# Optimization experiments

Measured on AMD Instinct MI355X. Metric: run time of the kernel, lower is better.

Reference implementation:

```python
import jax, jax.numpy as jnp
import numpy as np

B, N, D, H = 4, 2048, 512, 8
DK = D // H
NEG_SLOPE = 0.1


def setup_inputs() -> dict:
    key = jax.random.key(0)
    k_x, k_m, k_qkv, k_o, k_b = jax.random.split(key, 5)
    x = jax.random.normal(k_x, (B, N, D), dtype=jnp.float32)
    mask = jax.random.randint(k_m, (B, N, N), 0, 2).astype(bool)
    # guarantee self-edges so no row is fully masked (avoids NaN softmax)
    mask = mask | jnp.eye(N, dtype=bool)[None]
    scale = 1.0 / np.sqrt(D)
    Wqkv = jax.random.normal(k_qkv, (D, 3 * D), dtype=jnp.float32) * scale
    Wout = jax.random.normal(k_o, (D, D), dtype=jnp.float32) * scale
    bout = jax.random.normal(k_b, (D,), dtype=jnp.float32) * 0.01
    return {"x": x, "mask": mask, "Wqkv": Wqkv, "Wout": Wout, "bout": bout}


def reference(x, mask, Wqkv, Wout, bout):
    # x: (B,N,D), mask: (B,N,N) bool (True = keep edge)
    qkv = x @ Wqkv                               # (B,N,3D)
    q, k, v = jnp.split(qkv, 3, axis=-1)

    def heads(t):
        return t.reshape(B, N, H, DK).transpose(0, 2, 1, 3)  # (B,H,N,DK)

    q, k, v = heads(q), heads(k), heads(v)
    scores = jnp.einsum('bhnd,bhmd->bhnm', q, k) / np.sqrt(DK)  # (B,H,N,N)
    scores = jnp.where(mask[:, None], scores, -jnp.inf)
    attn = jax.nn.softmax(scores, axis=-1)
    out = jnp.einsum('bhnm,bhmd->bhnd', attn, v)               # (B,H,N,DK)
    out = out.transpose(0, 2, 1, 3).reshape(B, N, D)
    out = out @ Wout + bout
    return jnp.where(out >= 0, out, NEG_SLOPE * out)            # LeakyReLU
```

## Files before the change

kernel.cpp:

```cpp
#include <hip/hip_runtime.h>
#include <stdint.h>

#define Bb 4
#define Nn 2048
#define Dd 512
#define Hh 8
#define BN 8192

typedef __attribute__((ext_vector_type(4))) float f32x4;
typedef __attribute__((ext_vector_type(8))) short s16x8;

#define QSCALE 0.1803368801111204f

static constexpr size_t OFF_XB    = 1024;
static constexpr size_t OFF_WQKVT = OFF_XB    + (size_t)2 * BN * Dd;
static constexpr size_t OFF_WOUTT = OFF_WQKVT + (size_t)2 * 3 * Dd * Dd;
static constexpr size_t OFF_MASKP = OFF_WOUTT + (size_t)2 * Dd * Dd;
static constexpr size_t OFF_Q     = OFF_MASKP + (size_t)8 * Bb * Nn * (Nn / 64);
static constexpr size_t OFF_K     = OFF_Q     + (size_t)2 * BN * Dd;
static constexpr size_t OFF_VT    = OFF_K     + (size_t)2 * BN * Dd;
static constexpr size_t OFF_AO    = OFF_VT    + (size_t)2 * BN * Dd;

__device__ inline unsigned short f2bf(float f) {
  union { float f; unsigned int u; } v; v.f = f;
  const unsigned int u = v.u;
  return (unsigned short)((u + 0x7fffu + ((u >> 16) & 1u)) >> 16);
}

__device__ inline float exp2_hw(float x) {
  float r;
  asm("v_exp_f32 %0, %1" : "=v"(r) : "v"(x));
  return r;
}

__device__ inline unsigned int cvtpk_bf16(float lo, float hi) {
  unsigned int r;
  asm("v_cvt_pk_bf16_f32 %0, %1, %2" : "=v"(r) : "v"(lo), "v"(hi));
  return r;
}

__global__ void prep_kernel(const float* __restrict__ x, unsigned short* __restrict__ xb,
                            const float* __restrict__ Wqkv, unsigned short* __restrict__ wqkvT,
                            const float* __restrict__ Wout, unsigned short* __restrict__ woutT,
                            const unsigned char* __restrict__ mb, const int* __restrict__ mi,
                            unsigned long long* __restrict__ mp) {
  const int bid = blockIdx.x;
  if (bid < 2048) {
    for (int i = bid * 256 + threadIdx.x; i < BN * Dd / 4; i += 2048 * 256) {
      const float4 v = ((const float4*)x)[i];
      ushort4 o;
      o.x = f2bf(v.x); o.y = f2bf(v.y); o.z = f2bf(v.z); o.w = f2bf(v.w);
      ((ushort4*)xb)[i] = o;
    }
  } else if (bid < 3072) {
    for (int i = (bid - 2048) * 256 + threadIdx.x; i < Dd * 3 * Dd; i += 1024 * 256) {
      const int r = i / (3 * Dd), c = i - r * (3 * Dd);
      wqkvT[(size_t)c * Dd + r] = f2bf(Wqkv[i]);
    }
  } else if (bid < 3584) {
    for (int i = (bid - 3072) * 256 + threadIdx.x; i < Dd * Dd; i += 512 * 256) {
      const int r = i / Dd, c = i - r * Dd;
      woutT[(size_t)c * Dd + r] = f2bf(Wout[i]);
    }
  } else {
    const int lane = threadIdx.x & 63;
    const int ok = mb[(size_t)(lane + 1) * (Nn + 1)] != 0;
    const int bytemode = (__ballot(ok) == 0xFFFFFFFFFFFFFFFFull);
    const int nwords = Bb * Nn * (Nn / 64);
    int gw = ((bid - 3584) * 256 + threadIdx.x) >> 6;
    for (; gw < nwords; gw += 1024 * 4) {
      const size_t idx = (size_t)gw * 64 + lane;
      int v;
      if (bytemode) v = mb[idx]; else v = mi[idx];
      const unsigned long long bits = __ballot(v != 0);
      if (lane == 0) mp[gw] = bits;
    }
  }
}

template <int MODE>
__global__ __launch_bounds__(256, 2) void gemm128(
    const unsigned short* __restrict__ A,
    const unsigned short* __restrict__ BT,
    unsigned short* __restrict__ qb, unsigned short* __restrict__ kb,
    unsigned short* __restrict__ vt, const float* __restrict__ bias,
    float* __restrict__ outp) {
  __shared__ unsigned short Al[2][8192];
  __shared__ unsigned short Bl[2][8192];
  const int tid = threadIdx.x;
  const int lane = tid & 63, wv = tid >> 6;
  const int g = lane >> 4, n16 = lane & 15;
  const int m0 = blockIdx.x * 128;
  const int c0 = blockIdx.y * 128;
  const int wm = wv >> 1, wn = wv & 1;

  f32x4 acc[4][4] = {};

  auto stage = [&](int buf, int t) {
#pragma unroll
    for (int j = 0; j < 4; ++j) {
      const int base = (wv * 4 + j) * 1024;
      const int o = base + lane * 16;
      const int r = o >> 7;
      const int sl = ((o >> 4) & 7) ^ (r & 7);
      const unsigned short* ga = A + (size_t)(m0 + r) * 512 + t * 64 + sl * 8;
      __builtin_amdgcn_global_load_lds(
          (const __attribute__((address_space(1))) uint32_t*)ga,
          (__attribute__((address_space(3))) uint32_t*)&Al[buf][base / 2], 16, 0, 0);
      const unsigned short* gb = BT + (size_t)(c0 + r) * 512 + t * 64 + sl * 8;
      __builtin_amdgcn_global_load_lds(
          (const __attribute__((address_space(1))) uint32_t*)gb,
          (__attribute__((address_space(3))) uint32_t*)&Bl[buf][base / 2], 16, 0, 0);
    }
  };

  stage(0, 0);
  __syncthreads();
  int cur = 0;
  for (int t = 0; t < 8; ++t) {
    if (t < 7) stage(cur ^ 1, t + 1);
    s16x8 af[4][2], bfr[4][2];
#pragma unroll
    for (int f = 0; f < 4; ++f) {
#pragma unroll
      for (int kc = 0; kc < 2; ++kc) {
        const int rr = wm * 64 + f * 16 + n16;
        const int cc = wn * 64 + f * 16 + n16;
        const int sl = kc * 4 + g;
        af[f][kc]  = *(const s16x8*)&Al[cur][(rr * 128 + ((sl ^ (rr & 7)) * 16)) / 2];
        bfr[f][kc] = *(const s16x8*)&Bl[cur][(cc * 128 + ((sl ^ (cc & 7)) * 16)) / 2];
      }
    }
    __builtin_amdgcn_s_setprio(1);
#pragma unroll
    for (int i = 0; i < 4; ++i)
#pragma unroll
      for (int jn = 0; jn < 4; ++jn) {
        acc[i][jn] = __builtin_amdgcn_mfma_f32_16x16x32_bf16(af[i][0], bfr[jn][0], acc[i][jn], 0, 0, 0);
        acc[i][jn] = __builtin_amdgcn_mfma_f32_16x16x32_bf16(af[i][1], bfr[jn][1], acc[i][jn], 0, 0, 0);
      }
    __builtin_amdgcn_s_setprio(0);
    __syncthreads();
    cur ^= 1;
  }

  if (MODE == 0) {
#pragma unroll
    for (int i = 0; i < 4; ++i) {
      const int tok0 = m0 + wm * 64 + i * 16 + g * 4;
      const int bq = tok0 >> 11;
      const int nn0 = tok0 & 2047;
#pragma unroll
      for (int jn = 0; jn < 4; ++jn) {
        const int c = c0 + wn * 64 + jn * 16 + n16;
        if (c < 512) {
          const int h = c >> 6, dk = c & 63;
          unsigned short* qp = qb + (((size_t)bq * 8 + h) * 2048 + nn0) * 64 + dk;
#pragma unroll
          for (int r = 0; r < 4; ++r) qp[(size_t)r * 64] = f2bf(acc[i][jn][r] * QSCALE);
        } else if (c < 1024) {
          const int c2 = c - 512, h = c2 >> 6, dk = c2 & 63;
          unsigned short* kp = kb + (((size_t)bq * 8 + h) * 2048 + nn0) * 64 + dk;
#pragma unroll
          for (int r = 0; r < 4; ++r) kp[(size_t)r * 64] = f2bf(acc[i][jn][r]);
        } else {
          const int c2 = c - 1024, h = c2 >> 6, dk = c2 & 63;
          ushort4 pk;
          pk.x = f2bf(acc[i][jn][0]); pk.y = f2bf(acc[i][jn][1]);
          pk.z = f2bf(acc[i][jn][2]); pk.w = f2bf(acc[i][jn][3]);
          *(ushort4*)(vt + (((size_t)bq * 8 + h) * 64 + dk) * 2048 + nn0) = pk;
        }
      }
    }
  } else {
#pragma unroll
    for (int jn = 0; jn < 4; ++jn) {
      const int c = c0 + wn * 64 + jn * 16 + n16;
      const float bc = bias[c];
#pragma unroll
      for (int i = 0; i < 4; ++i) {
        const int tok0 = m0 + wm * 64 + i * 16 + g * 4;
#pragma unroll
        for (int r = 0; r < 4; ++r) {
          float v = acc[i][jn][r] + bc;
          v = v >= 0.f ? v : 0.1f * v;
          outp[(size_t)(tok0 + r) * 512 + c] = v;
        }
      }
    }
  }
}

__global__ __launch_bounds__(256, 4) void attn_kernel(
    const unsigned short* __restrict__ qb, const unsigned short* __restrict__ kb,
    const unsigned short* __restrict__ vt, const unsigned long long* __restrict__ mp,
    unsigned short* __restrict__ ao) {
  __shared__ unsigned short Kl[2][4096];
  __shared__ unsigned short Vl[2][4096];
  __shared__ unsigned short Pl[4][1024];
  const int tid = threadIdx.x, lane = tid & 63, wv = tid >> 6;
  const int g = lane >> 4, n16 = lane & 15;
  const int sbid = (blockIdx.x & 7) * 128 + (blockIdx.x >> 3);
  const int qt = sbid & 31, bh = sbid >> 5;
  const int b = bh >> 3, h = bh & 7;
  const int n0 = qt * 64 + wv * 16;
  const unsigned short* Qh = qb + (size_t)bh * 2048 * 64;
  const unsigned short* Kh = kb + (size_t)bh * 2048 * 64;
  const unsigned short* Vh = vt + (size_t)bh * 64 * 2048;
  const unsigned long long* mrow = mp + ((size_t)b * 2048 + n0 + n16) * 32;

  const s16x8 qf0 = *(const s16x8*)&Qh[(size_t)(n0 + n16) * 64 + g * 8];
  const s16x8 qf1 = *(const s16x8*)&Qh[(size_t)(n0 + n16) * 64 + 32 + g * 8];

  const s16x8 ones = {0x3F80, 0x3F80, 0x3F80, 0x3F80, 0x3F80, 0x3F80, 0x3F80, 0x3F80};

  f32x4 of[4] = {};
  f32x4 acc_l = {};

  unsigned short* Pw = Pl[wv];
  int pwo[4], pro[2];
#pragma unroll
  for (int mf = 0; mf < 4; ++mf) {
    int bo = n16 * 128 + mf * 32 + g * 8;
    pwo[mf] = bo ^ ((n16 & 7) << 4);
  }
#pragma unroll
  for (int kc = 0; kc < 2; ++kc) {
    int bo = n16 * 128 + kc * 64 + g * 16;
    pro[kc] = bo ^ ((n16 & 7) << 4);
  }

  auto stage = [&](int buf, int m0) {
#pragma unroll
    for (int j = 0; j < 2; ++j) {
      const int base = (wv * 2 + j) * 1024;
      const int o = base + lane * 16;
      const int r = o >> 7;
      const int sl = ((o >> 4) & 7) ^ (r & 7);
      const unsigned short* gk = Kh + (size_t)(m0 + r) * 64 + sl * 8;
      __builtin_amdgcn_global_load_lds(
          (const __attribute__((address_space(1))) uint32_t*)gk,
          (__attribute__((address_space(3))) uint32_t*)&Kl[buf][base / 2], 16, 0, 0);
      const unsigned short* gv = Vh + (size_t)r * 2048 + m0 + sl * 8;
      __builtin_amdgcn_global_load_lds(
          (const __attribute__((address_space(1))) uint32_t*)gv,
          (__attribute__((address_space(3))) uint32_t*)&Vl[buf][base / 2], 16, 0, 0);
    }
  };

  stage(0, 0);
  unsigned long long wbits = mrow[0];
  __syncthreads();
  int cur = 0;
  for (int it = 0; it < 32; ++it) {
    if (it < 31) stage(cur ^ 1, (it + 1) * 64);
    const unsigned long long wnext = (it < 31) ? mrow[it + 1] : 0ull;

    f32x4 sc[4] = {};
    __builtin_amdgcn_s_setprio(1);
#pragma unroll
    for (int mf = 0; mf < 4; ++mf) {
      const int ml = mf * 16 + n16;
#pragma unroll
      for (int kc = 0; kc < 2; ++kc) {
        const int sl = kc * 4 + g;
        const s16x8 kf = *(const s16x8*)&Kl[cur][(ml * 128 + ((sl ^ (ml & 7)) * 16)) / 2];
        sc[mf] = __builtin_amdgcn_mfma_f32_16x16x32_bf16(kf, kc ? qf1 : qf0, sc[mf], 0, 0, 0);
      }
    }
    __builtin_amdgcn_s_setprio(0);

    const unsigned int wlo = (unsigned int)(wbits >> (g * 4));
    const unsigned int whi = (unsigned int)(wbits >> (32 + g * 4));

    unsigned int w[8];
#pragma unroll
    for (int mf = 0; mf < 4; ++mf) {
      const unsigned int wsel = (mf & 2) ? whi : wlo;
      float p[4];
#pragma unroll
      for (int r = 0; r < 4; ++r) {
        const int bit = ((mf & 1) ? 16 : 0) + r;
        float pv = exp2_hw(sc[mf][r]);
        p[r] = (wsel & (1u << bit)) ? pv : 0.0f;
      }
      w[mf * 2]     = cvtpk_bf16(p[0], p[1]);
      w[mf * 2 + 1] = cvtpk_bf16(p[2], p[3]);
    }

#pragma unroll
    for (int mf = 0; mf < 4; ++mf) {
      uint2 pk2; pk2.x = w[mf * 2]; pk2.y = w[mf * 2 + 1];
      *(uint2*)((char*)Pw + pwo[mf]) = pk2;
    }
    __builtin_amdgcn_s_setprio(1);
#pragma unroll
    for (int kc = 0; kc < 2; ++kc) {
      const s16x8 pf = *(const s16x8*)((const char*)Pw + pro[kc]);
      acc_l = __builtin_amdgcn_mfma_f32_16x16x32_bf16(pf, ones, acc_l, 0, 0, 0);
#pragma unroll
      for (int df = 0; df < 4; ++df) {
        const int dk = df * 16 + n16;
        const int sl = kc * 4 + g;
        const s16x8 vf = *(const s16x8*)&Vl[cur][(dk * 128 + ((sl ^ (dk & 7)) * 16)) / 2];
        of[df] = __builtin_amdgcn_mfma_f32_16x16x32_bf16(pf, vf, of[df], 0, 0, 0);
      }
    }
    __builtin_amdgcn_s_setprio(0);
    wbits = wnext;
    __syncthreads();
    cur ^= 1;
  }

  float rinv[4];
#pragma unroll
  for (int r = 0; r < 4; ++r) rinv[r] = 1.f / acc_l[r];
#pragma unroll
  for (int df = 0; df < 4; ++df)
#pragma unroll
    for (int r = 0; r < 4; ++r) {
      const int token = b * 2048 + n0 + 4 * g + r;
      ao[(size_t)token * 512 + h * 64 + df * 16 + n16] = f2bf(of[df][r] * rinv[r]);
    }
}

extern "C" void kernel_launch(void* const* d_in, const int* in_sizes, int n_in,
                              void* d_out, int out_size, void* d_ws, size_t ws_size,
                              hipStream_t stream) {
  const float* x = (const float*)d_in[0];
  const void* mask = d_in[1];
  const float* Wqkv = (const float*)d_in[2];
  const float* Wout = (const float*)d_in[3];
  const float* bout = (const float*)d_in[4];
  float* out = (float*)d_out;
  char* ws = (char*)d_ws;

  unsigned short* xb = (unsigned short*)(ws + OFF_XB);
  unsigned short* wqkvT = (unsigned short*)(ws + OFF_WQKVT);
  unsigned short* woutT = (unsigned short*)(ws + OFF_WOUTT);
  unsigned long long* mp = (unsigned long long*)(ws + OFF_MASKP);
  unsigned short* qb = (unsigned short*)(ws + OFF_Q);
  unsigned short* kb = (unsigned short*)(ws + OFF_K);
  unsigned short* vt = (unsigned short*)(ws + OFF_VT);
  unsigned short* ao = (unsigned short*)(ws + OFF_AO);

  prep_kernel<<<4608, 256, 0, stream>>>(x, xb, Wqkv, wqkvT, Wout, woutT,
                                        (const unsigned char*)mask, (const int*)mask, mp);
  gemm128<0><<<dim3(64, 12), 256, 0, stream>>>(xb, wqkvT, qb, kb, vt, nullptr, nullptr);
  attn_kernel<<<1024, 256, 0, stream>>>(qb, kb, vt, mp, ao);
  gemm128<1><<<dim3(64, 4), 256, 0, stream>>>(ao, woutT, nullptr, nullptr, nullptr, bout, out);
}
```

Before: 129.7 us.

## Tile weight transposes via LDS, stage V-transpose epilogue, narrow out-proj tiles

```diff
diff --git a/kernel.cpp b/kernel.cpp
--- a/kernel.cpp
+++ b/kernel.cpp
@@ -39,35 +39,60 @@
   return r;
 }
 
+__device__ inline void gload16(const void* g, void* l) {
+  __builtin_amdgcn_global_load_lds(
+      (const __attribute__((address_space(1))) uint32_t*)g,
+      (__attribute__((address_space(3))) uint32_t*)l, 16, 0, 0);
+}
+
 __global__ void prep_kernel(const float* __restrict__ x, unsigned short* __restrict__ xb,
                             const float* __restrict__ Wqkv, unsigned short* __restrict__ wqkvT,
                             const float* __restrict__ Wout, unsigned short* __restrict__ woutT,
                             const unsigned char* __restrict__ mb, const int* __restrict__ mi,
                             unsigned long long* __restrict__ mp) {
-  const int bid = blockIdx.x;
+  __shared__ float tsm[64][65];
+  const int bid = blockIdx.x, tid = threadIdx.x;
   if (bid < 2048) {
-    for (int i = bid * 256 + threadIdx.x; i < BN * Dd / 4; i += 2048 * 256) {
+    for (int i = bid * 256 + tid; i < BN * Dd / 4; i += 2048 * 256) {
       const float4 v = ((const float4*)x)[i];
       ushort4 o;
       o.x = f2bf(v.x); o.y = f2bf(v.y); o.z = f2bf(v.z); o.w = f2bf(v.w);
       ((ushort4*)xb)[i] = o;
     }
-  } else if (bid < 3072) {
-    for (int i = (bid - 2048) * 256 + threadIdx.x; i < Dd * 3 * Dd; i += 1024 * 256) {
-      const int r = i / (3 * Dd), c = i - r * (3 * Dd);
-      wqkvT[(size_t)c * Dd + r] = f2bf(Wqkv[i]);
-    }
-  } else if (bid < 3584) {
-    for (int i = (bid - 3072) * 256 + threadIdx.x; i < Dd * Dd; i += 512 * 256) {
-      const int r = i / Dd, c = i - r * Dd;
-      woutT[(size_t)c * Dd + r] = f2bf(Wout[i]);
+  } else if (bid < 2304) {
+    const float* W; unsigned short* WT; int C, tt;
+    if (bid < 2240) { W = Wqkv; WT = wqkvT; C = 1536; tt = bid - 2048; }
+    else            { W = Wout; WT = woutT; C = 512;  tt = bid - 2240; }
+    const int tcols = C >> 6;
+    const int rt = tt / tcols, ct = tt - rt * tcols;
+    const int r0 = rt * 64, c0t = ct * 64;
+    {
+      const int row = tid >> 4, colq = tid & 15;
+#pragma unroll
+      for (int rr = 0; rr < 4; ++rr) {
+        const float4 v = *(const float4*)&W[(size_t)(r0 + rr * 16 + row) * C + c0t + colq * 4];
+        tsm[rr * 16 + row][colq * 4 + 0] = v.x;
+        tsm[rr * 16 + row][colq * 4 + 1] = v.y;
+        tsm[rr * 16 + row][colq * 4 + 2] = v.z;
+        tsm[rr * 16 + row][colq * 4 + 3] = v.w;
+      }
+    }
+    __syncthreads();
+    {
+      const int ocl = tid >> 2, seg = tid & 3;
+      unsigned short ob[16];
+#pragma unroll
+      for (int j = 0; j < 16; ++j) ob[j] = f2bf(tsm[seg * 16 + j][ocl]);
+      unsigned short* dst = WT + (size_t)(c0t + ocl) * 512 + r0 + seg * 16;
+      *(s16x8*)dst = *(s16x8*)ob;
+      *(s16x8*)(dst + 8) = *(s16x8*)(ob + 8);
     }
   } else {
-    const int lane = threadIdx.x & 63;
+    const int lane = tid & 63;
     const int ok = mb[(size_t)(lane + 1) * (Nn + 1)] != 0;
     const int bytemode = (__ballot(ok) == 0xFFFFFFFFFFFFFFFFull);
     const int nwords = Bb * Nn * (Nn / 64);
-    int gw = ((bid - 3584) * 256 + threadIdx.x) >> 6;
+    int gw = ((bid - 2304) * 256 + tid) >> 6;
     for (; gw < nwords; gw += 1024 * 4) {
       const size_t idx = (size_t)gw * 64 + lane;
       int v;
@@ -78,23 +103,24 @@
   }
 }
 
-template <int MODE>
+template <int MODE, int BNt>
 __global__ __launch_bounds__(256, 2) void gemm128(
     const unsigned short* __restrict__ A,
     const unsigned short* __restrict__ BT,
     unsigned short* __restrict__ qb, unsigned short* __restrict__ kb,
     unsigned short* __restrict__ vt, const float* __restrict__ bias,
     float* __restrict__ outp) {
-  __shared__ unsigned short Al[2][8192];
-  __shared__ unsigned short Bl[2][8192];
+  constexpr int JN = BNt / 32;
+  constexpr int BBYTES = BNt * 128;
+  __shared__ char smem[32768 + 2 * BBYTES];
   const int tid = threadIdx.x;
   const int lane = tid & 63, wv = tid >> 6;
   const int g = lane >> 4, n16 = lane & 15;
   const int m0 = blockIdx.x * 128;
-  const int c0 = blockIdx.y * 128;
+  const int c0 = blockIdx.y * BNt;
   const int wm = wv >> 1, wn = wv & 1;
 
-  f32x4 acc[4][4] = {};
+  f32x4 acc[4][JN] = {};
 
   auto stage = [&](int buf, int t) {
 #pragma unroll
@@ -103,14 +129,15 @@
       const int o = base + lane * 16;
       const int r = o >> 7;
       const int sl = ((o >> 4) & 7) ^ (r & 7);
-      const unsigned short* ga = A + (size_t)(m0 + r) * 512 + t * 64 + sl * 8;
-      __builtin_amdgcn_global_load_lds(
-          (const __attribute__((address_space(1))) uint32_t*)ga,
-          (__attribute__((address_space(3))) uint32_t*)&Al[buf][base / 2], 16, 0, 0);
-      const unsigned short* gb = BT + (size_t)(c0 + r) * 512 + t * 64 + sl * 8;
-      __builtin_amdgcn_global_load_lds(
-          (const __attribute__((address_space(1))) uint32_t*)gb,
-          (__attribute__((address_space(3))) uint32_t*)&Bl[buf][base / 2], 16, 0, 0);
+      gload16(A + (size_t)(m0 + r) * 512 + t * 64 + sl * 8, smem + buf * 16384 + base);
+    }
+#pragma unroll
+    for (int j = 0; j < BNt / 32; ++j) {
+      const int base = (wv * (BNt / 32) + j) * 1024;
+      const int o = base + lane * 16;
+      const int r = o >> 7;
+      const int sl = ((o >> 4) & 7) ^ (r & 7);
+      gload16(BT + (size_t)(c0 + r) * 512 + t * 64 + sl * 8, smem + 32768 + buf * BBYTES + base);
     }
   };
 
@@ -119,23 +146,30 @@
   int cur = 0;
   for (int t = 0; t < 8; ++t) {
     if (t < 7) stage(cur ^ 1, t + 1);
-    s16x8 af[4][2], bfr[4][2];
-#pragma unroll
-    for (int f = 0; f < 4; ++f) {
+    const unsigned short* Ab = (const unsigned short*)(smem + cur * 16384);
+    const unsigned short* Bbuf = (const unsigned short*)(smem + 32768 + cur * BBYTES);
+    s16x8 af[4][2], bfr[JN][2];
+#pragma unroll
+    for (int f = 0; f < 4; ++f)
 #pragma unroll
       for (int kc = 0; kc < 2; ++kc) {
         const int rr = wm * 64 + f * 16 + n16;
-        const int cc = wn * 64 + f * 16 + n16;
         const int sl = kc * 4 + g;
-        af[f][kc]  = *(const s16x8*)&Al[cur][(rr * 128 + ((sl ^ (rr & 7)) * 16)) / 2];
-        bfr[f][kc] = *(const s16x8*)&Bl[cur][(cc * 128 + ((sl ^ (cc & 7)) * 16)) / 2];
-      }
-    }
+        af[f][kc] = *(const s16x8*)&Ab[(rr * 128 + ((sl ^ (rr & 7)) * 16)) / 2];
+      }
+#pragma unroll
+    for (int f = 0; f < JN; ++f)
+#pragma unroll
+      for (int kc = 0; kc < 2; ++kc) {
+        const int cc = wn * (BNt / 2) + f * 16 + n16;
+        const int sl = kc * 4 + g;
+        bfr[f][kc] = *(const s16x8*)&Bbuf[(cc * 128 + ((sl ^ (cc & 7)) * 16)) / 2];
+      }
     __builtin_amdgcn_s_setprio(1);
 #pragma unroll
     for (int i = 0; i < 4; ++i)
 #pragma unroll
-      for (int jn = 0; jn < 4; ++jn) {
+      for (int jn = 0; jn < JN; ++jn) {
         acc[i][jn] = __builtin_amdgcn_mfma_f32_16x16x32_bf16(af[i][0], bfr[jn][0], acc[i][jn], 0, 0, 0);
         acc[i][jn] = __builtin_amdgcn_mfma_f32_16x16x32_bf16(af[i][1], bfr[jn][1], acc[i][jn], 0, 0, 0);
       }
@@ -145,37 +179,57 @@
   }
 
   if (MODE == 0) {
-#pragma unroll
-    for (int i = 0; i < 4; ++i) {
-      const int tok0 = m0 + wm * 64 + i * 16 + g * 4;
-      const int bq = tok0 >> 11;
-      const int nn0 = tok0 & 2047;
-#pragma unroll
-      for (int jn = 0; jn < 4; ++jn) {
-        const int c = c0 + wn * 64 + jn * 16 + n16;
-        if (c < 512) {
-          const int h = c >> 6, dk = c & 63;
-          unsigned short* qp = qb + (((size_t)bq * 8 + h) * 2048 + nn0) * 64 + dk;
-#pragma unroll
-          for (int r = 0; r < 4; ++r) qp[(size_t)r * 64] = f2bf(acc[i][jn][r] * QSCALE);
-        } else if (c < 1024) {
-          const int c2 = c - 512, h = c2 >> 6, dk = c2 & 63;
-          unsigned short* kp = kb + (((size_t)bq * 8 + h) * 2048 + nn0) * 64 + dk;
-#pragma unroll
-          for (int r = 0; r < 4; ++r) kp[(size_t)r * 64] = f2bf(acc[i][jn][r]);
-        } else {
-          const int c2 = c - 1024, h = c2 >> 6, dk = c2 & 63;
+    const int bq = m0 >> 11, nn0 = m0 & 2047;
+    if (c0 < 1024) {
+#pragma unroll
+      for (int i = 0; i < 4; ++i) {
+        const int tl0 = wm * 64 + i * 16 + g * 4;
+#pragma unroll
+        for (int jn = 0; jn < JN; ++jn) {
+          const int c = c0 + wn * 64 + jn * 16 + n16;
+          if (c < 512) {
+            const int h = c >> 6, dk = c & 63;
+            unsigned short* qp = qb + (((size_t)bq * 8 + h) * 2048 + nn0 + tl0) * 64 + dk;
+#pragma unroll
+            for (int r = 0; r < 4; ++r) qp[(size_t)r * 64] = f2bf(acc[i][jn][r] * QSCALE);
+          } else {
+            const int c2 = c - 512, h = c2 >> 6, dk = c2 & 63;
+            unsigned short* kp = kb + (((size_t)bq * 8 + h) * 2048 + nn0 + tl0) * 64 + dk;
+#pragma unroll
+            for (int r = 0; r < 4; ++r) kp[(size_t)r * 64] = f2bf(acc[i][jn][r]);
+          }
+        }
+      }
+    } else {
+      constexpr int SW = 136;
+      unsigned short* Ep = (unsigned short*)smem;
+#pragma unroll
+      for (int i = 0; i < 4; ++i) {
+        const int tl0 = wm * 64 + i * 16 + g * 4;
+#pragma unroll
+        for (int jn = 0; jn < JN; ++jn) {
+          const int cl = wn * 64 + jn * 16 + n16;
           ushort4 pk;
           pk.x = f2bf(acc[i][jn][0]); pk.y = f2bf(acc[i][jn][1]);
           pk.z = f2bf(acc[i][jn][2]); pk.w = f2bf(acc[i][jn][3]);
-          *(ushort4*)(vt + (((size_t)bq * 8 + h) * 64 + dk) * 2048 + nn0) = pk;
+          *(ushort4*)&Ep[cl * SW + (tl0 ^ (((cl >> 3) & 7) << 3))] = pk;
         }
       }
+      __syncthreads();
+#pragma unroll
+      for (int itc = 0; itc < 8; ++itc) {
+        const int chunk = itc * 256 + tid;
+        const int cl = chunk >> 4, tc = chunk & 15;
+        const s16x8 v = *(const s16x8*)&Ep[cl * SW + ((tc * 8) ^ (((cl >> 3) & 7) << 3))];
+        const int c2 = c0 + cl - 1024;
+        const int h = c2 >> 6, dk = c2 & 63;
+        *(s16x8*)(vt + (((size_t)bq * 8 + h) * 64 + dk) * 2048 + nn0 + tc * 8) = v;
+      }
     }
   } else {
 #pragma unroll
-    for (int jn = 0; jn < 4; ++jn) {
-      const int c = c0 + wn * 64 + jn * 16 + n16;
+    for (int jn = 0; jn < JN; ++jn) {
+      const int c = c0 + wn * (BNt / 2) + jn * 16 + n16;
       const float bc = bias[c];
 #pragma unroll
       for (int i = 0; i < 4; ++i) {
@@ -237,14 +291,8 @@
       const int o = base + lane * 16;
       const int r = o >> 7;
       const int sl = ((o >> 4) & 7) ^ (r & 7);
-      const unsigned short* gk = Kh + (size_t)(m0 + r) * 64 + sl * 8;
-      __builtin_amdgcn_global_load_lds(
-          (const __attribute__((address_space(1))) uint32_t*)gk,
-          (__attribute__((address_space(3))) uint32_t*)&Kl[buf][base / 2], 16, 0, 0);
-      const unsigned short* gv = Vh + (size_t)r * 2048 + m0 + sl * 8;
-      __builtin_amdgcn_global_load_lds(
-          (const __attribute__((address_space(1))) uint32_t*)gv,
-          (__attribute__((address_space(3))) uint32_t*)&Vl[buf][base / 2], 16, 0, 0);
+      gload16(Kh + (size_t)(m0 + r) * 64 + sl * 8, (char*)&Kl[buf][0] + base);
+      gload16(Vh + (size_t)r * 2048 + m0 + sl * 8, (char*)&Vl[buf][0] + base);
     }
   };
 
@@ -276,13 +324,13 @@
     unsigned int w[8];
 #pragma unroll
     for (int mf = 0; mf < 4; ++mf) {
-      const unsigned int wsel = (mf & 2) ? whi : wlo;
+      const unsigned int wsel = ((mf & 2) ? whi : wlo) >> ((mf & 1) * 16);
       float p[4];
 #pragma unroll
       for (int r = 0; r < 4; ++r) {
-        const int bit = ((mf & 1) ? 16 : 0) + r;
-        float pv = exp2_hw(sc[mf][r]);
-        p[r] = (wsel & (1u << bit)) ? pv : 0.0f;
+        const unsigned int sm = (unsigned int)__builtin_amdgcn_sbfe((int)wsel, r, 1);
+        const float pv = exp2_hw(sc[mf][r]);
+        p[r] = __uint_as_float(__float_as_uint(pv) & sm);
       }
       w[mf * 2]     = cvtpk_bf16(p[0], p[1]);
       w[mf * 2 + 1] = cvtpk_bf16(p[2], p[3]);
@@ -344,9 +392,9 @@
   unsigned short* vt = (unsigned short*)(ws + OFF_VT);
   unsigned short* ao = (unsigned short*)(ws + OFF_AO);
 
-  prep_kernel<<<4608, 256, 0, stream>>>(x, xb, Wqkv, wqkvT, Wout, woutT,
+  prep_kernel<<<3328, 256, 0, stream>>>(x, xb, Wqkv, wqkvT, Wout, woutT,
                                         (const unsigned char*)mask, (const int*)mask, mp);
-  gemm128<0><<<dim3(64, 12), 256, 0, stream>>>(xb, wqkvT, qb, kb, vt, nullptr, nullptr);
+  gemm128<0, 128><<<dim3(64, 12), 256, 0, stream>>>(xb, wqkvT, qb, kb, vt, nullptr, nullptr);
   attn_kernel<<<1024, 256, 0, stream>>>(qb, kb, vt, mp, ao);
-  gemm128<1><<<dim3(64, 4), 256, 0, stream>>>(ao, woutT, nullptr, nullptr, nullptr, bout, out);
-}
+  gemm128<1, 64><<<dim3(64, 8), 256, 0, stream>>>(ao, woutT, nullptr, nullptr, nullptr, bout, out);
+}
```

Result: faster. 123.3 us (-4.9%).
